# Performance work log

Measured on AMD Instinct MI355X. Metric: run time of the kernel, lower is better.

## Reference

```python
import jax, jax.numpy as jnp
import numpy as np

N = 100_000          # nodes
E = 1_600_000        # edges (avg degree 16)
FEAT = 128           # num_features
HID = 128            # hidden_dim
CLS = 10             # num_classes
G = 4                # grid_size (num RBF grids)
L = 3                # gnn_layers
NG = 64              # number of graphs in batch
GRID_MIN, GRID_MAX = -2.0, 2.0
DENOM = (GRID_MAX - GRID_MIN) / (G - 1)
GRID = jnp.linspace(GRID_MIN, GRID_MAX, G)
LN_EPS = 1e-5


def _layernorm(x, scale, bias):
    m = jnp.mean(x, axis=-1, keepdims=True)
    v = jnp.var(x, axis=-1, keepdims=True)
    return (x - m) * jax.lax.rsqrt(v + LN_EPS) * scale + bias


def _fkan(x, ln_s, ln_b, sW, sb, bW, bb):
    # FastKANLayer: spline_linear(rbf(layernorm(x)).flatten) + base_linear(silu(x))
    z = _layernorm(x, ln_s, ln_b)
    basis = jnp.exp(-(((z[..., None] - GRID) / DENOM) ** 2))      # [n, in, G]
    spline = basis.reshape(x.shape[0], -1) @ sW.T + sb            # [n, out]
    base = jax.nn.silu(x) @ bW.T + bb                             # [n, out]
    return spline + base


def setup_inputs() -> dict:
    key = jax.random.key(0)
    ks = jax.random.split(key, 20)
    inp = {
        "x": jax.random.normal(ks[0], (N, FEAT), dtype=jnp.float32),
        "edge_index": jax.random.randint(ks[1], (2, E), 0, N, dtype=jnp.int64 if jax.config.jax_enable_x64 else jnp.int32),
        "batch": jnp.sort(jax.random.randint(ks[2], (N,), 0, NG)),
        # per-GCN-layer FKAN params (in=out=128 for all 3 layers)
        "ln_s": jnp.ones((L, FEAT), jnp.float32),
        "ln_b": jnp.zeros((L, FEAT), jnp.float32),
        "sW": jax.random.normal(ks[3], (L, HID, FEAT * G), jnp.float32) * 0.05,
        "sb": jnp.zeros((L, HID), jnp.float32),
        "bW": jax.random.normal(ks[4], (L, HID, FEAT), jnp.float32) * 0.05,
        "bb": jnp.zeros((L, HID), jnp.float32),
        "gcn_b": jnp.zeros((L, HID), jnp.float32),
        # readout FastKAN: single FastKANLayer 128 -> 10
        "ro_ln_s": jnp.ones((HID,), jnp.float32),
        "ro_ln_b": jnp.zeros((HID,), jnp.float32),
        "ro_sW": jax.random.normal(ks[5], (CLS, HID * G), jnp.float32) * 0.05,
        "ro_sb": jnp.zeros((CLS,), jnp.float32),
        "ro_bW": jax.random.normal(ks[6], (CLS, HID), jnp.float32) * 0.05,
        "ro_bb": jnp.zeros((CLS,), jnp.float32),
    }
    return inp


def reference(x, edge_index, batch, ln_s, ln_b, sW, sb, bW, bb, gcn_b,
              ro_ln_s, ro_ln_b, ro_sW, ro_sb, ro_bW, ro_bb):
    n = x.shape[0]
    loops = jnp.arange(n, dtype=edge_index.dtype)
    src = jnp.concatenate([edge_index[0], loops])   # with self-loops (GCNConv default)
    dst = jnp.concatenate([edge_index[1], loops])
    deg = jax.ops.segment_sum(jnp.ones_like(src, dtype=x.dtype), dst, num_segments=n)
    dinv = jnp.where(deg > 0, jax.lax.rsqrt(deg), 0.0)
    norm = dinv[src] * dinv[dst]                    # [E+N]

    for i in range(L):
        h = _fkan(x, ln_s[i], ln_b[i], sW[i], sb[i], bW[i], bb[i])    # KAN transform
        agg = jax.ops.segment_sum(norm[:, None] * h[src], dst, num_segments=n)
        x = jax.nn.silu(agg + gcn_b[i])             # dropout p=0 -> identity

    cnt = jax.ops.segment_sum(jnp.ones((n,), x.dtype), batch, num_segments=NG)
    pooled = jax.ops.segment_sum(x, batch, num_segments=NG) / jnp.maximum(cnt, 1.0)[:, None]
    out = _fkan(pooled, ro_ln_s, ro_ln_b, ro_sW, ro_sb, ro_bW, ro_bb)
    return jax.nn.log_softmax(out, axis=1)
```

## Files before the change

### kernel.cpp

```cpp
#include <hip/hip_runtime.h>
#include <math.h>

#define NN     100000
#define NE     1600000
#define FEAT   128
#define GQ     4
#define NL     3
#define NGR    64
#define NCLS   10
#define KSPL   512
#define NKS    10
#define BM     32
#define NB     1563
#define NCHUNK 256
#define CHUNK  6250
#define TILE   1024
#define NT     ((NN + TILE - 1) / TILE)
#define WSTRIDE (NKS*8*2*512)

typedef __attribute__((ext_vector_type(8))) short short8;
typedef __attribute__((ext_vector_type(4))) float floatx4;
typedef __attribute__((ext_vector_type(4))) uint uintx4;

__device__ __forceinline__ float fsilu(float x){ return x / (1.f + __expf(-x)); }
__device__ __forceinline__ ushort f2bf(float f){
  uint u = __builtin_bit_cast(uint, f);
  return (ushort)((u + 0x7FFFu + ((u >> 16) & 1u)) >> 16);
}
__device__ __forceinline__ float bf2f(ushort h){ return __builtin_bit_cast(float, ((uint)h) << 16); }
__device__ __forceinline__ uint bu(float f){ return __builtin_bit_cast(uint, f); }
__device__ __forceinline__ uint pkbf(float lo, float hi){
  return __builtin_amdgcn_perm(bu(hi), bu(lo), 0x07060302u);
}

__global__ __launch_bounds__(256) void k_zero_i(int* __restrict__ p, int n){
  int i = blockIdx.x*256 + threadIdx.x; if (i < n) p[i] = 0;
}
__global__ __launch_bounds__(256) void k_zero_f(float* __restrict__ p, int n){
  int i = blockIdx.x*256 + threadIdx.x; if (i < n) p[i] = 0.f;
}
__global__ __launch_bounds__(256) void k_hist(const int* __restrict__ dst, int* __restrict__ hist, int ne){
  int e = blockIdx.x*256 + threadIdx.x; if (e < ne) atomicAdd(&hist[dst[e]], 1);
}

__global__ __launch_bounds__(256) void k_scan_a(const int* __restrict__ hist, int* __restrict__ tsum){
  __shared__ int red[4];
  const int base = blockIdx.x * TILE;
  int s = 0;
  #pragma unroll
  for (int j = 0; j < 4; ++j){
    int idx = base + threadIdx.x + j*256;
    if (idx < NN) s += hist[idx];
  }
  #pragma unroll
  for (int off = 32; off; off >>= 1) s += __shfl_down(s, off);
  if ((threadIdx.x & 63) == 0) red[threadIdx.x >> 6] = s;
  __syncthreads();
  if (threadIdx.x == 0) tsum[blockIdx.x] = red[0] + red[1] + red[2] + red[3];
}

__global__ __launch_bounds__(128) void k_scan_b(const int* __restrict__ tsum,
                                                int* __restrict__ toff, int* __restrict__ rpN){
  __shared__ int lds[128];
  const int tid = threadIdx.x;
  int v = (tid < NT) ? tsum[tid] : 0;
  lds[tid] = v; __syncthreads();
  for (int off = 1; off < 128; off <<= 1){
    int u = (tid >= off) ? lds[tid - off] : 0;
    __syncthreads();
    lds[tid] += u;
    __syncthreads();
  }
  if (tid < NT) toff[tid] = lds[tid] - v;
  if (tid == NT - 1) *rpN = lds[tid];
}

__global__ __launch_bounds__(256) void k_scan_c(const int* __restrict__ hist,
                                                const int* __restrict__ toff,
                                                int* __restrict__ rp,
                                                float* __restrict__ dinv){
  __shared__ int lds[256];
  const int tid = threadIdx.x;
  const int base = blockIdx.x * TILE + tid*4;
  int h[4]; int s = 0;
  #pragma unroll
  for (int j = 0; j < 4; ++j){ int idx = base + j; h[j] = (idx < NN) ? hist[idx] : 0; s += h[j]; }
  lds[tid] = s; __syncthreads();
  for (int off = 1; off < 256; off <<= 1){
    int u = (tid >= off) ? lds[tid - off] : 0;
    __syncthreads();
    lds[tid] += u;
    __syncthreads();
  }
  int run = toff[blockIdx.x] + lds[tid] - s;
  #pragma unroll
  for (int j = 0; j < 4; ++j){
    int idx = base + j;
    if (idx < NN){
      rp[idx] = run; run += h[j];
      dinv[idx] = rsqrtf((float)h[j] + 1.f);
    }
  }
}

__global__ __launch_bounds__(256) void k_binA(const int* __restrict__ src, const int* __restrict__ dst,
                                              uint* __restrict__ priv, int* __restrict__ seg){
  __shared__ int hist[NB];
  __shared__ int cur[NB];
  __shared__ int scanbuf[256];
  const int c = blockIdx.x, tid = threadIdx.x;
  const size_t e0 = (size_t)c * CHUNK;
  for (int i = tid; i < NB; i += 256) hist[i] = 0;
  __syncthreads();
  for (int i = tid; i < CHUNK; i += 256) atomicAdd(&hist[dst[e0+i] >> 6], 1);
  __syncthreads();
  int loc[7]; int s = 0;
  const int base = tid * 7;
  #pragma unroll
  for (int j = 0; j < 7; ++j){ int idx = base+j; int v = (idx < NB) ? hist[idx] : 0; loc[j] = s; s += v; }
  scanbuf[tid] = s;
  __syncthreads();
  for (int off = 1; off < 256; off <<= 1){
    int u = (tid >= off) ? scanbuf[tid-off] : 0;
    __syncthreads();
    scanbuf[tid] += u;
    __syncthreads();
  }
  const int run = scanbuf[tid] - s;
  #pragma unroll
  for (int j = 0; j < 7; ++j){
    int idx = base+j;
    if (idx < NB){ int st = run + loc[j]; seg[c*(NB+1)+idx] = st; cur[idx] = st; }
  }
  if (tid == 0) seg[c*(NB+1)+NB] = CHUNK;
  __syncthreads();
  for (int i = tid; i < CHUNK; i += 256){
    const uint ss = (uint)src[e0+i], dd = (uint)dst[e0+i];
    const int p = atomicAdd(&cur[dd >> 6], 1);
    priv[(size_t)c*CHUNK + p] = (ss << 6) | (dd & 63u);
  }
}

__global__ __launch_bounds__(256) void k_gathE2(const uint* __restrict__ priv, const int* __restrict__ seg,
                                                const int* __restrict__ rp, int* __restrict__ col){
  __shared__ int cur[64];
  const int b = blockIdx.x, tid = threadIdx.x;
  const int n0 = b * 64;
  if (tid < 64){
    const int idx = n0 + tid;
    cur[tid] = rp[(idx < NN) ? idx : NN];
  }
  __syncthreads();
  const int c = tid;
  const int s0 = seg[c*(NB+1) + b], s1 = seg[c*(NB+1) + b + 1];
  const size_t pbase = (size_t)c*CHUNK;
  for (int i = s0; i < s1; ++i){
    const uint e = priv[pbase + i];
    const int p = atomicAdd(&cur[e & 63u], 1);
    col[p] = (int)(e >> 6);
  }
}

__global__ __launch_bounds__(256) void k_wprep(const float* __restrict__ sW, const float* __restrict__ bW,
                                               ushort* __restrict__ wimg){
  int idx = blockIdx.x*256 + threadIdx.x;
  if (idx >= NL*WSTRIDE) return;
  const int j    = idx & 7;
  const int lane = (idx >> 3) & 63;
  const int ks   = (idx >> 9) & 1;
  const int nr   = (idx >> 10) & 7;
  const int qq   = (idx >> 13) % NKS;
  const int l    = idx / (NKS << 13);
  const int colc = nr*16 + (lane & 15);
  const int kg   = qq*64 + ks*32 + (lane >> 4)*8 + j;
  const float v  = (kg < KSPL) ? sW[((size_t)l*FEAT + colc)*KSPL + kg]
                               : bW[((size_t)l*FEAT + colc)*FEAT + (kg - KSPL)];
  wimg[idx] = f2bf(v);
}

template <typename TIn>
__global__ __launch_bounds__(128) void k_fkan(
    const TIn* __restrict__ xin,
    const ushort* __restrict__ wimg,
    const float* __restrict__ ln_s, const float* __restrict__ ln_b,
    const float* __restrict__ sb, const float* __restrict__ bb,
    const float* __restrict__ dinv,
    ushort* __restrict__ hprime)
{
  __shared__ char xb[BM*256];
  __shared__ float lnS[128], lnB[128], sbias[128];

  const int tid  = threadIdx.x;
  const int lane = tid & 63, wv = tid >> 6;
  const int node0 = blockIdx.x * BM;

  lnS[tid] = ln_s[tid]; lnB[tid] = ln_b[tid]; sbias[tid] = sb[tid] + bb[tid];

  const int lm = tid >> 2, part = tid & 3;
  const int node = node0 + lm;
  const uint swl = ((uint)(lm & 7)) << 4;
  char* xrow_w = xb + lm*256;
  float s1 = 0.f, s2 = 0.f;
  if constexpr (sizeof(TIn) == 4){
    const float4* xr = (const float4*)((const float*)xin + (size_t)node*FEAT + part*32);
    #pragma unroll
    for (int j = 0; j < 4; ++j){
      const float4 a = xr[2*j], b = xr[2*j+1];
      s1 += a.x+a.y+a.z+a.w + b.x+b.y+b.z+b.w;
      s2 += a.x*a.x+a.y*a.y+a.z*a.z+a.w*a.w + b.x*b.x+b.y*b.y+b.z*b.z+b.w*b.w;
      uintx4 pk;
      pk.x = pkbf(a.x, a.y); pk.y = pkbf(a.z, a.w);
      pk.z = pkbf(b.x, b.y); pk.w = pkbf(b.z, b.w);
      *(uintx4*)(xrow_w + (((uint)(part*64 + j*16)) ^ swl)) = pk;
    }
  } else {
    const uintx4* xr = (const uintx4*)((const ushort*)xin + (size_t)node*FEAT + part*32);
    #pragma unroll
    for (int j = 0; j < 4; ++j){
      const uintx4 v = xr[j];
      #pragma unroll
      for (int w = 0; w < 4; ++w){
        const float f0 = bf2f((ushort)(v[w] & 0xffff)), f1 = bf2f((ushort)(v[w] >> 16));
        s1 += f0 + f1; s2 += f0*f0 + f1*f1;
      }
      *(uintx4*)(xrow_w + (((uint)(part*64 + j*16)) ^ swl)) = v;
    }
  }
  s1 += __shfl_xor(s1, 1); s2 += __shfl_xor(s2, 1);
  s1 += __shfl_xor(s1, 2); s2 += __shfl_xor(s2, 2);
  const float mean = s1 * (1.f/128.f);
  const float var  = s2 * (1.f/128.f) - mean*mean;
  const float rsv  = rsqrtf(var + 1e-5f);
  __syncthreads();

  const int l15 = lane & 15, l4h = lane >> 4;
  const int row = wv*16 + l15;
  const uint swz = ((uint)(row & 7)) << 4;
  const char* xrow = xb + row*256;
  const float mrow = __shfl(mean, (lane & 15) << 2);
  const float rrow = __shfl(rsv,  (lane & 15) << 2);

  floatx4 acc[8];
  #pragma unroll
  for (int nr = 0; nr < 8; ++nr){ floatx4 z4 = {0.f,0.f,0.f,0.f}; acc[nr] = z4; }

  const short8* w8 = (const short8*)wimg;

  auto afrag = [&](int sp)->short8 {
    const int q = sp >> 1, ks = sp & 1;
    if (q < 8){
      const int f0 = q*16 + ks*8 + l4h*2;
      const uint xx = *(const uint*)(xrow + (((uint)(f0*2)) ^ swz));
      const float x0 = bf2f((ushort)(xx & 0xffff)), x1 = bf2f((ushort)(xx >> 16));
      const float2 ls = *(const float2*)(lnS + f0);
      const float2 lb = *(const float2*)(lnB + f0);
      const float z0 = (x0 - mrow)*rrow*ls.x + lb.x;
      const float z1 = (x1 - mrow)*rrow*ls.y + lb.y;
      float e0[4], e1[4];
      #pragma unroll
      for (int g = 0; g < 4; ++g){
        const float gc = -2.f + (4.f/3.f)*(float)g;
        const float t0 = (z0 - gc)*0.75f;
        const float t1 = (z1 - gc)*0.75f;
        e0[g] = __expf(-t0*t0);
        e1[g] = __expf(-t1*t1);
      }
      uintx4 pw;
      pw.x = pkbf(e0[0], e0[1]); pw.y = pkbf(e0[2], e0[3]);
      pw.z = pkbf(e1[0], e1[1]); pw.w = pkbf(e1[2], e1[3]);
      return __builtin_bit_cast(short8, pw);
    } else {
      const int f0 = (q - 8)*64 + ks*32 + l4h*8;
      const uintx4 xx = *(const uintx4*)(xrow + (((uint)(f0*2)) ^ swz));
      uintx4 pw;
      #pragma unroll
      for (int w = 0; w < 4; ++w){
        const float x0 = bf2f((ushort)(xx[w] & 0xffff)), x1 = bf2f((ushort)(xx[w] >> 16));
        pw[w] = pkbf(fsilu(x0), fsilu(x1));
      }
      return __builtin_bit_cast(short8, pw);
    }
  };

  short8 b0[8], b1[8];
  #pragma unroll
  for (int nr = 0; nr < 8; ++nr) b0[nr] = w8[(size_t)(nr*2)*64 + lane];

  #pragma unroll
  for (int sp = 0; sp < 20; sp += 2){
    {
      const int q1 = (sp + 1) >> 1, ks1 = (sp + 1) & 1;
      #pragma unroll
      for (int nr = 0; nr < 8; ++nr) b1[nr] = w8[(size_t)(q1*16 + nr*2 + ks1)*64 + lane];
    }
    {
      const short8 af = afrag(sp);
      #pragma unroll
      for (int nr = 0; nr < 8; ++nr)
        acc[nr] = __builtin_amdgcn_mfma_f32_16x16x32_bf16(af, b0[nr], acc[nr], 0, 0, 0);
    }
    if (sp + 2 < 20){
      const int q2 = (sp + 2) >> 1, ks2 = (sp + 2) & 1;
      #pragma unroll
      for (int nr = 0; nr < 8; ++nr) b0[nr] = w8[(size_t)(q2*16 + nr*2 + ks2)*64 + lane];
    }
    {
      const short8 af = afrag(sp + 1);
      #pragma unroll
      for (int nr = 0; nr < 8; ++nr)
        acc[nr] = __builtin_amdgcn_mfma_f32_16x16x32_bf16(af, b1[nr], acc[nr], 0, 0, 0);
    }
  }

  const int rbase = node0 + wv*16 + l4h*4;
  float dvv[4];
  #pragma unroll
  for (int j = 0; j < 4; ++j) dvv[j] = dinv[rbase + j];
  #pragma unroll
  for (int nr = 0; nr < 8; ++nr){
    const int cf = nr*16 + l15;
    const float sv = sbias[cf];
    #pragma unroll
    for (int j = 0; j < 4; ++j)
      hprime[(size_t)(rbase + j)*FEAT + cf] = f2bf(dvv[j]*(acc[nr][j] + sv));
  }
}

__global__ __launch_bounds__(256) void k_aggD(
    const ushort* __restrict__ hprime, const int* __restrict__ rp,
    const int* __restrict__ col, const float* __restrict__ dinv,
    const float* __restrict__ gb, ushort* __restrict__ xout)
{
  const int wv = threadIdx.x >> 6, lane = threadIdx.x & 63;
  const int d = blockIdx.x*4 + wv;
  if (d >= NN) return;
  const uint* h2 = (const uint*)hprime;
  const uint v = h2[(size_t)d*64 + lane];
  float a0 = bf2f((ushort)(v & 0xffff)), a1 = bf2f((ushort)(v >> 16));
  const int j0 = rp[d], j1 = rp[d+1];
  int j = j0;
  for (; j + 7 < j1; j += 8){
    uint w[8];
    #pragma unroll
    for (int u = 0; u < 8; ++u) w[u] = h2[(size_t)col[j+u]*64 + lane];
    #pragma unroll
    for (int u = 0; u < 8; ++u){
      a0 += bf2f((ushort)(w[u] & 0xffff));
      a1 += bf2f((ushort)(w[u] >> 16));
    }
  }
  for (; j + 3 < j1; j += 4){
    uint w[4];
    #pragma unroll
    for (int u = 0; u < 4; ++u) w[u] = h2[(size_t)col[j+u]*64 + lane];
    #pragma unroll
    for (int u = 0; u < 4; ++u){
      a0 += bf2f((ushort)(w[u] & 0xffff));
      a1 += bf2f((ushort)(w[u] >> 16));
    }
  }
  for (; j < j1; ++j){
    const uint w = h2[(size_t)col[j]*64 + lane];
    a0 += bf2f((ushort)(w & 0xffff)); a1 += bf2f((ushort)(w >> 16));
  }
  const float dv = dinv[d];
  const float2 b2 = *(const float2*)(gb + 2*lane);
  a0 = fsilu(dv*a0 + b2.x);
  a1 = fsilu(dv*a1 + b2.y);
  ((uint*)xout)[(size_t)d*64 + lane] = (uint)f2bf(a0) | ((uint)f2bf(a1) << 16);
}

__global__ __launch_bounds__(128) void k_pool(const ushort* __restrict__ x,
                                              const int* __restrict__ batch,
                                              float* __restrict__ pooled,
                                              float* __restrict__ cnt, int n){
  const int f = threadIdx.x;
  const int start = blockIdx.x * 64;
  const int end   = min(start + 64, n);
  if (start >= end) return;
  int cur = batch[start];
  float acc = 0.f, c = 0.f;
  for (int i = start; i < end; ++i){
    const int b = batch[i];
    if (b != cur){
      atomicAdd(&pooled[(size_t)cur*FEAT + f], acc);
      if (f == 0) atomicAdd(&cnt[cur], c);
      cur = b; acc = 0.f; c = 0.f;
    }
    acc += bf2f(x[(size_t)i*FEAT + f]);
    c += 1.f;
  }
  atomicAdd(&pooled[(size_t)cur*FEAT + f], acc);
  if (f == 0) atomicAdd(&cnt[cur], c);
}

__global__ __launch_bounds__(128) void k_pool_div(float* __restrict__ pooled,
                                                  const float* __restrict__ cnt){
  const int g = blockIdx.x, f = threadIdx.x;
  pooled[(size_t)g*FEAT + f] /= fmaxf(cnt[g], 1.f);
}

__global__ __launch_bounds__(128) void k_readout(const float* __restrict__ pooled,
    const float* __restrict__ ln_s, const float* __restrict__ ln_b,
    const float* __restrict__ sW, const float* __restrict__ sb,
    const float* __restrict__ bW, const float* __restrict__ bb,
    float* __restrict__ out){
  __shared__ float cb[KSPL + FEAT];
  __shared__ float wred[2][2];
  __shared__ float outv[NCLS];
  const int tid = threadIdx.x, lane = tid & 63, wave = tid >> 6;
  const int g = blockIdx.x;

  const float xvv = pooled[(size_t)g*FEAT + tid];
  float s1 = xvv, s2 = xvv*xvv;
  #pragma unroll
  for (int off = 32; off; off >>= 1){ s1 += __shfl_down(s1, off); s2 += __shfl_down(s2, off); }
  if (lane == 0){ wred[wave][0] = s1; wred[wave][1] = s2; }
  __syncthreads();
  const float m   = (wred[0][0] + wred[1][0]) * (1.f/FEAT);
  const float var = (wred[0][1] + wred[1][1]) * (1.f/FEAT) - m*m;
  const float rs  = rsqrtf(var + 1e-5f);
  const float z   = (xvv - m) * rs * ln_s[tid] + ln_b[tid];
  #pragma unroll
  for (int gg = 0; gg < GQ; ++gg){
    const float t = (z - (-2.f + (4.f/3.f)*(float)gg)) * 0.75f;
    cb[tid*GQ + gg] = __expf(-t*t);
  }
  cb[KSPL + tid] = fsilu(xvv);
  __syncthreads();

  if (tid < NCLS){
    const float* wr = sW + (size_t)tid*KSPL;
    const float* br = bW + (size_t)tid*FEAT;
    float acc = sb[tid] + bb[tid];
    for (int k = 0; k < KSPL; ++k) acc += cb[k] * wr[k];
    for (int k = 0; k < FEAT; ++k) acc += cb[KSPL + k] * br[k];
    outv[tid] = acc;
  }
  __syncthreads();
  if (tid == 0){
    float mx = -1e30f;
    for (int o = 0; o < NCLS; ++o) mx = fmaxf(mx, outv[o]);
    float se = 0.f;
    for (int o = 0; o < NCLS; ++o) se += __expf(outv[o] - mx);
    const float lse = mx + logf(se);
    for (int o = 0; o < NCLS; ++o) out[(size_t)g*NCLS + o] = outv[o] - lse;
  }
}

extern "C" void kernel_launch(void* const* d_in, const int* in_sizes, int n_in,
                              void* d_out, int out_size, void* d_ws, size_t ws_size,
                              hipStream_t stream) {
  const float* x     = (const float*)d_in[0];
  const int*   edge  = (const int*)d_in[1];
  const int*   batch = (const int*)d_in[2];
  const float* ln_s  = (const float*)d_in[3];
  const float* ln_b  = (const float*)d_in[4];
  const float* sW    = (const float*)d_in[5];
  const float* sb    = (const float*)d_in[6];
  const float* bW    = (const float*)d_in[7];
  const float* bb    = (const float*)d_in[8];
  const float* gcn_b = (const float*)d_in[9];
  const float* ro_ln_s = (const float*)d_in[10];
  const float* ro_ln_b = (const float*)d_in[11];
  const float* ro_sW   = (const float*)d_in[12];
  const float* ro_sb   = (const float*)d_in[13];
  const float* ro_bW   = (const float*)d_in[14];
  const float* ro_bb   = (const float*)d_in[15];
  float* out = (float*)d_out;

  const int* src = edge;
  const int* dst = edge + NE;

  char* W = (char*)d_ws;
  size_t off = 0;
  auto alloc = [&](size_t bytes){ size_t r = off; off += (bytes + 1023) & ~((size_t)1023); return r; };
  float*  dinv   = (float*) (W + alloc((size_t)NN*4));
  ushort* wimg   = (ushort*)(W + alloc((size_t)NL*WSTRIDE*2));
  int*    hist   = (int*)   (W + alloc((size_t)NN*4));
  int*    rp     = (int*)   (W + alloc((size_t)(NN+1)*4));
  int*    tsum   = (int*)   (W + alloc((size_t)NT*4));
  int*    toff   = (int*)   (W + alloc((size_t)NT*4));
  uint*   priv   = (uint*)  (W + alloc((size_t)NE*4));
  int*    seg    = (int*)   (W + alloc((size_t)NCHUNK*(NB+1)*4));
  int*    col    = (int*)   (W + alloc((size_t)NE*4));
  ushort* hprime = (ushort*)(W + alloc((size_t)NN*FEAT*2));
  ushort* xcur   = (ushort*)(W + alloc((size_t)NN*FEAT*2));
  float*  pooled = (float*) (W + alloc((size_t)(NGR*FEAT + NGR)*4));
  float*  cnt    = pooled + NGR*FEAT;

  k_zero_i<<<(NN+255)/256, 256, 0, stream>>>(hist, NN);
  k_zero_f<<<(NGR*FEAT+NGR+255)/256, 256, 0, stream>>>(pooled, NGR*FEAT + NGR);
  k_hist<<<(NE+255)/256, 256, 0, stream>>>(dst, hist, NE);
  k_scan_a<<<NT, 256, 0, stream>>>(hist, tsum);
  k_scan_b<<<1, 128, 0, stream>>>(tsum, toff, rp + NN);
  k_scan_c<<<NT, 256, 0, stream>>>(hist, toff, rp, dinv);
  k_binA<<<NCHUNK, 256, 0, stream>>>(src, dst, priv, seg);
  k_gathE2<<<NB, 256, 0, stream>>>(priv, seg, rp, col);
  k_wprep<<<(NL*WSTRIDE + 255)/256, 256, 0, stream>>>(sW, bW, wimg);

  const int fkan_grid = NN / BM;
  for (int l = 0; l < NL; ++l){
    const ushort* wl = wimg + (size_t)l*WSTRIDE;
    if (l == 0)
      k_fkan<float><<<fkan_grid, 128, 0, stream>>>(x, wl,
          ln_s + l*FEAT, ln_b + l*FEAT, sb + l*FEAT, bb + l*FEAT, dinv, hprime);
    else
      k_fkan<ushort><<<fkan_grid, 128, 0, stream>>>(xcur, wl,
          ln_s + l*FEAT, ln_b + l*FEAT, sb + l*FEAT, bb + l*FEAT, dinv, hprime);
    k_aggD<<<(NN+3)/4, 256, 0, stream>>>(hprime, rp, col, dinv, gcn_b + l*FEAT, xcur);
  }

  k_pool<<<(NN+63)/64, 128, 0, stream>>>(xcur, batch, pooled, cnt, NN);
  k_pool_div<<<NGR, 128, 0, stream>>>(pooled, cnt);
  k_readout<<<NGR, 128, 0, stream>>>(pooled, ro_ln_s, ro_ln_b,
                                     ro_sW, ro_sb, ro_bW, ro_bb, out);
}
```

Measured before the change: 490.3 us.

## Stage FKAN weight fragments in LDS via async global_load_lds with larger node tiles

The FKAN kernel now processes 64 nodes per block with 256 threads. Each wave previously loaded all weight fragments from global memory on its own; now the block loads them cooperatively into a double-buffered LDS stage using global_load_lds, and every wave reads them from LDS. The goal is to cut redundant global and L2 weight traffic and to share it across four waves. The cost is a __syncthreads on every k-step and an unrolled loop that has become a rolled one, which may serialize the MFMA pipeline. Bounds checks are added for the partial last tile.

```diff
diff --git a/kernel.cpp b/kernel.cpp
--- a/kernel.cpp
+++ b/kernel.cpp
@@ -10,7 +10,7 @@
 #define NCLS   10
 #define KSPL   512
 #define NKS    10
-#define BM     32
+#define BM     64
 #define NB     1563
 #define NCHUNK 256
 #define CHUNK  6250
@@ -31,6 +31,11 @@
 __device__ __forceinline__ uint bu(float f){ return __builtin_bit_cast(uint, f); }
 __device__ __forceinline__ uint pkbf(float lo, float hi){
   return __builtin_amdgcn_perm(bu(hi), bu(lo), 0x07060302u);
+}
+__device__ __forceinline__ void gld_lds16(const ushort* g, ushort* l){
+  __builtin_amdgcn_global_load_lds(
+      (const __attribute__((address_space(1))) uint*)g,
+      (__attribute__((address_space(3))) uint*)l, 16, 0, 0);
 }
 
 __global__ __launch_bounds__(256) void k_zero_i(int* __restrict__ p, int n){
@@ -179,7 +184,7 @@
 }
 
 template <typename TIn>
-__global__ __launch_bounds__(128) void k_fkan(
+__global__ __launch_bounds__(256) void k_fkan(
     const TIn* __restrict__ xin,
     const ushort* __restrict__ wimg,
     const float* __restrict__ ln_s, const float* __restrict__ ln_b,
@@ -188,63 +193,87 @@
     ushort* __restrict__ hprime)
 {
   __shared__ char xb[BM*256];
+  __shared__ ushort Bst[2][8*512];
   __shared__ float lnS[128], lnB[128], sbias[128];
 
   const int tid  = threadIdx.x;
   const int lane = tid & 63, wv = tid >> 6;
   const int node0 = blockIdx.x * BM;
 
-  lnS[tid] = ln_s[tid]; lnB[tid] = ln_b[tid]; sbias[tid] = sb[tid] + bb[tid];
+  if (tid < 128){ lnS[tid] = ln_s[tid]; lnB[tid] = ln_b[tid]; sbias[tid] = sb[tid] + bb[tid]; }
 
   const int lm = tid >> 2, part = tid & 3;
   const int node = node0 + lm;
   const uint swl = ((uint)(lm & 7)) << 4;
   char* xrow_w = xb + lm*256;
   float s1 = 0.f, s2 = 0.f;
-  if constexpr (sizeof(TIn) == 4){
-    const float4* xr = (const float4*)((const float*)xin + (size_t)node*FEAT + part*32);
-    #pragma unroll
-    for (int j = 0; j < 4; ++j){
-      const float4 a = xr[2*j], b = xr[2*j+1];
-      s1 += a.x+a.y+a.z+a.w + b.x+b.y+b.z+b.w;
-      s2 += a.x*a.x+a.y*a.y+a.z*a.z+a.w*a.w + b.x*b.x+b.y*b.y+b.z*b.z+b.w*b.w;
-      uintx4 pk;
-      pk.x = pkbf(a.x, a.y); pk.y = pkbf(a.z, a.w);
-      pk.z = pkbf(b.x, b.y); pk.w = pkbf(b.z, b.w);
-      *(uintx4*)(xrow_w + (((uint)(part*64 + j*16)) ^ swl)) = pk;
+  if (node < NN){
+    if constexpr (sizeof(TIn) == 4){
+      const float4* xr = (const float4*)((const float*)xin + (size_t)node*FEAT + part*32);
+      #pragma unroll
+      for (int j = 0; j < 4; ++j){
+        const float4 a = xr[2*j], b = xr[2*j+1];
+        s1 += a.x+a.y+a.z+a.w + b.x+b.y+b.z+b.w;
+        s2 += a.x*a.x+a.y*a.y+a.z*a.z+a.w*a.w + b.x*b.x+b.y*b.y+b.z*b.z+b.w*b.w;
+        uintx4 pk;
+        pk.x = pkbf(a.x, a.y); pk.y = pkbf(a.z, a.w);
+        pk.z = pkbf(b.x, b.y); pk.w = pkbf(b.z, b.w);
+        *(uintx4*)(xrow_w + (((uint)(part*64 + j*16)) ^ swl)) = pk;
+      }
+    } else {
+      const uintx4* xr = (const uintx4*)((const ushort*)xin + (size_t)node*FEAT + part*32);
+      #pragma unroll
+      for (int j = 0; j < 2; ++j){
+        const uintx4 v = xr[j];
+        #pragma unroll
+        for (int w = 0; w < 4; ++w){
+          const float f0 = bf2f((ushort)(v[w] & 0xffff)), f1 = bf2f((ushort)(v[w] >> 16));
+          s1 += f0 + f1; s2 += f0*f0 + f1*f1;
+        }
+        *(uintx4*)(xrow_w + (((uint)(part*64 + j*16)) ^ swl)) = v;
+      }
+      #pragma unroll
+      for (int j = 2; j < 4; ++j){
+        const uintx4 v = xr[j];
+        #pragma unroll
+        for (int w = 0; w < 4; ++w){
+          const float f0 = bf2f((ushort)(v[w] & 0xffff)), f1 = bf2f((ushort)(v[w] >> 16));
+          s1 += f0 + f1; s2 += f0*f0 + f1*f1;
+        }
+        *(uintx4*)(xrow_w + (((uint)(part*64 + j*16)) ^ swl)) = v;
+      }
     }
   } else {
-    const uintx4* xr = (const uintx4*)((const ushort*)xin + (size_t)node*FEAT + part*32);
-    #pragma unroll
-    for (int j = 0; j < 4; ++j){
-      const uintx4 v = xr[j];
-      #pragma unroll
-      for (int w = 0; w < 4; ++w){
-        const float f0 = bf2f((ushort)(v[w] & 0xffff)), f1 = bf2f((ushort)(v[w] >> 16));
-        s1 += f0 + f1; s2 += f0*f0 + f1*f1;
-      }
-      *(uintx4*)(xrow_w + (((uint)(part*64 + j*16)) ^ swl)) = v;
-    }
+    uintx4 z4 = {0u,0u,0u,0u};
+    #pragma unroll
+    for (int j = 0; j < 4; ++j)
+      *(uintx4*)(xrow_w + (((uint)(part*64 + j*16)) ^ swl)) = z4;
   }
   s1 += __shfl_xor(s1, 1); s2 += __shfl_xor(s2, 1);
   s1 += __shfl_xor(s1, 2); s2 += __shfl_xor(s2, 2);
   const float mean = s1 * (1.f/128.f);
   const float var  = s2 * (1.f/128.f) - mean*mean;
   const float rsv  = rsqrtf(var + 1e-5f);
+
+  {
+    #pragma unroll
+    for (int f = 0; f < 2; ++f){
+      const int nr = (wv << 1) | f;
+      gld_lds16(wimg + ((size_t)(nr*2) << 9) + (lane << 3), &Bst[0][nr << 9]);
+    }
+  }
   __syncthreads();
 
   const int l15 = lane & 15, l4h = lane >> 4;
   const int row = wv*16 + l15;
   const uint swz = ((uint)(row & 7)) << 4;
   const char* xrow = xb + row*256;
-  const float mrow = __shfl(mean, (lane & 15) << 2);
-  const float rrow = __shfl(rsv,  (lane & 15) << 2);
+  const float mrow = __shfl(mean, l15 << 2);
+  const float rrow = __shfl(rsv,  l15 << 2);
 
   floatx4 acc[8];
   #pragma unroll
   for (int nr = 0; nr < 8; ++nr){ floatx4 z4 = {0.f,0.f,0.f,0.f}; acc[nr] = z4; }
-
-  const short8* w8 = (const short8*)wimg;
 
   auto afrag = [&](int sp)->short8 {
     const int q = sp >> 1, ks = sp & 1;
@@ -282,47 +311,41 @@
     }
   };
 
-  short8 b0[8], b1[8];
-  #pragma unroll
-  for (int nr = 0; nr < 8; ++nr) b0[nr] = w8[(size_t)(nr*2)*64 + lane];
-
-  #pragma unroll
-  for (int sp = 0; sp < 20; sp += 2){
-    {
+  for (int sp = 0; sp < 20; ++sp){
+    if (sp + 1 < 20){
       const int q1 = (sp + 1) >> 1, ks1 = (sp + 1) & 1;
       #pragma unroll
-      for (int nr = 0; nr < 8; ++nr) b1[nr] = w8[(size_t)(q1*16 + nr*2 + ks1)*64 + lane];
-    }
-    {
-      const short8 af = afrag(sp);
-      #pragma unroll
-      for (int nr = 0; nr < 8; ++nr)
-        acc[nr] = __builtin_amdgcn_mfma_f32_16x16x32_bf16(af, b0[nr], acc[nr], 0, 0, 0);
-    }
-    if (sp + 2 < 20){
-      const int q2 = (sp + 2) >> 1, ks2 = (sp + 2) & 1;
-      #pragma unroll
-      for (int nr = 0; nr < 8; ++nr) b0[nr] = w8[(size_t)(q2*16 + nr*2 + ks2)*64 + lane];
-    }
-    {
-      const short8 af = afrag(sp + 1);
-      #pragma unroll
-      for (int nr = 0; nr < 8; ++nr)
-        acc[nr] = __builtin_amdgcn_mfma_f32_16x16x32_bf16(af, b1[nr], acc[nr], 0, 0, 0);
-    }
+      for (int f = 0; f < 2; ++f){
+        const int nr = (wv << 1) | f;
+        gld_lds16(wimg + ((size_t)(q1*16 + nr*2 + ks1) << 9) + (lane << 3),
+                  &Bst[(sp + 1) & 1][nr << 9]);
+      }
+    }
+    const short8 af = afrag(sp);
+    const char* bb_ = (const char*)&Bst[sp & 1][0];
+    short8 bf[8];
+    #pragma unroll
+    for (int nr = 0; nr < 8; ++nr)
+      bf[nr] = *(const short8*)(bb_ + (nr << 10) + (lane << 4));
+    #pragma unroll
+    for (int nr = 0; nr < 8; ++nr)
+      acc[nr] = __builtin_amdgcn_mfma_f32_16x16x32_bf16(af, bf[nr], acc[nr], 0, 0, 0);
+    __syncthreads();
   }
 
   const int rbase = node0 + wv*16 + l4h*4;
   float dvv[4];
   #pragma unroll
-  for (int j = 0; j < 4; ++j) dvv[j] = dinv[rbase + j];
+  for (int j = 0; j < 4; ++j) dvv[j] = (rbase + j < NN) ? dinv[rbase + j] : 0.f;
   #pragma unroll
   for (int nr = 0; nr < 8; ++nr){
     const int cf = nr*16 + l15;
     const float sv = sbias[cf];
     #pragma unroll
-    for (int j = 0; j < 4; ++j)
-      hprime[(size_t)(rbase + j)*FEAT + cf] = f2bf(dvv[j]*(acc[nr][j] + sv));
+    for (int j = 0; j < 4; ++j){
+      const int r = rbase + j;
+      if (r < NN) hprime[(size_t)r*FEAT + cf] = f2bf(dvv[j]*(acc[nr][j] + sv));
+    }
   }
 }
 
@@ -499,14 +522,14 @@
   k_gathE2<<<NB, 256, 0, stream>>>(priv, seg, rp, col);
   k_wprep<<<(NL*WSTRIDE + 255)/256, 256, 0, stream>>>(sW, bW, wimg);
 
-  const int fkan_grid = NN / BM;
+  const int fkan_grid = (NN + BM - 1) / BM;
   for (int l = 0; l < NL; ++l){
     const ushort* wl = wimg + (size_t)l*WSTRIDE;
     if (l == 0)
-      k_fkan<float><<<fkan_grid, 128, 0, stream>>>(x, wl,
+      k_fkan<float><<<fkan_grid, 256, 0, stream>>>(x, wl,
           ln_s + l*FEAT, ln_b + l*FEAT, sb + l*FEAT, bb + l*FEAT, dinv, hprime);
     else
-      k_fkan<ushort><<<fkan_grid, 128, 0, stream>>>(xcur, wl,
+      k_fkan<ushort><<<fkan_grid, 256, 0, stream>>>(xcur, wl,
           ln_s + l*FEAT, ln_b + l*FEAT, sb + l*FEAT, bb + l*FEAT, dinv, hprime);
     k_aggD<<<(NN+3)/4, 256, 0, stream>>>(hprime, rp, col, dinv, gcn_b + l*FEAT, xcur);
   }
```

Measured after the change: 507.6 us. +3.5%, slower.

## Split FKAN GEMM columns across four waves per block and use exp2 for RBF

Applied to the files above, without the earlier changes.

The FKAN kernel block grows from 128 to 256 threads. Each pair of waves now shares a 16-row tile and splits the 128 output columns in half, so each wave holds 4 accumulators and 4 weight fragments instead of 8. Row LayerNorm statistics now go through shared memory instead of lane shuffles. The RBF exponent folds the scale and log2(e) into one constant and calls exp2f. In exchange, each pair of waves computes the A fragments (basis and silu) twice, which is meant to be offset by lower register pressure and higher occupancy.

```diff
diff --git a/kernel.cpp b/kernel.cpp
--- a/kernel.cpp
+++ b/kernel.cpp
@@ -179,7 +179,7 @@
 }
 
 template <typename TIn>
-__global__ __launch_bounds__(128) void k_fkan(
+__global__ __launch_bounds__(256) void k_fkan(
     const TIn* __restrict__ xin,
     const ushort* __restrict__ wimg,
     const float* __restrict__ ln_s, const float* __restrict__ ln_b,
@@ -188,63 +188,69 @@
     ushort* __restrict__ hprime)
 {
   __shared__ char xb[BM*256];
+  __shared__ float2 rstat[BM];
   __shared__ float lnS[128], lnB[128], sbias[128];
 
   const int tid  = threadIdx.x;
   const int lane = tid & 63, wv = tid >> 6;
   const int node0 = blockIdx.x * BM;
 
-  lnS[tid] = ln_s[tid]; lnB[tid] = ln_b[tid]; sbias[tid] = sb[tid] + bb[tid];
-
-  const int lm = tid >> 2, part = tid & 3;
+  if (tid < 128){ lnS[tid] = ln_s[tid]; lnB[tid] = ln_b[tid]; sbias[tid] = sb[tid] + bb[tid]; }
+
+  const int lm = tid >> 3, part = tid & 7;
   const int node = node0 + lm;
   const uint swl = ((uint)(lm & 7)) << 4;
   char* xrow_w = xb + lm*256;
   float s1 = 0.f, s2 = 0.f;
   if constexpr (sizeof(TIn) == 4){
-    const float4* xr = (const float4*)((const float*)xin + (size_t)node*FEAT + part*32);
-    #pragma unroll
-    for (int j = 0; j < 4; ++j){
+    const float4* xr = (const float4*)((const float*)xin + (size_t)node*FEAT + part*16);
+    #pragma unroll
+    for (int j = 0; j < 2; ++j){
       const float4 a = xr[2*j], b = xr[2*j+1];
       s1 += a.x+a.y+a.z+a.w + b.x+b.y+b.z+b.w;
       s2 += a.x*a.x+a.y*a.y+a.z*a.z+a.w*a.w + b.x*b.x+b.y*b.y+b.z*b.z+b.w*b.w;
       uintx4 pk;
       pk.x = pkbf(a.x, a.y); pk.y = pkbf(a.z, a.w);
       pk.z = pkbf(b.x, b.y); pk.w = pkbf(b.z, b.w);
-      *(uintx4*)(xrow_w + (((uint)(part*64 + j*16)) ^ swl)) = pk;
+      *(uintx4*)(xrow_w + (((uint)(part*32 + j*16)) ^ swl)) = pk;
     }
   } else {
-    const uintx4* xr = (const uintx4*)((const ushort*)xin + (size_t)node*FEAT + part*32);
-    #pragma unroll
-    for (int j = 0; j < 4; ++j){
+    const uintx4* xr = (const uintx4*)((const ushort*)xin + (size_t)node*FEAT + part*16);
+    #pragma unroll
+    for (int j = 0; j < 2; ++j){
       const uintx4 v = xr[j];
       #pragma unroll
       for (int w = 0; w < 4; ++w){
         const float f0 = bf2f((ushort)(v[w] & 0xffff)), f1 = bf2f((ushort)(v[w] >> 16));
         s1 += f0 + f1; s2 += f0*f0 + f1*f1;
       }
-      *(uintx4*)(xrow_w + (((uint)(part*64 + j*16)) ^ swl)) = v;
+      *(uintx4*)(xrow_w + (((uint)(part*32 + j*16)) ^ swl)) = v;
     }
   }
   s1 += __shfl_xor(s1, 1); s2 += __shfl_xor(s2, 1);
   s1 += __shfl_xor(s1, 2); s2 += __shfl_xor(s2, 2);
-  const float mean = s1 * (1.f/128.f);
-  const float var  = s2 * (1.f/128.f) - mean*mean;
-  const float rsv  = rsqrtf(var + 1e-5f);
+  s1 += __shfl_xor(s1, 4); s2 += __shfl_xor(s2, 4);
+  if (part == 0){
+    const float mean = s1 * (1.f/128.f);
+    const float var  = s2 * (1.f/128.f) - mean*mean;
+    rstat[lm] = make_float2(mean, rsqrtf(var + 1e-5f));
+  }
   __syncthreads();
 
   const int l15 = lane & 15, l4h = lane >> 4;
-  const int row = wv*16 + l15;
+  const int rg = wv >> 1, wn = wv & 1;
+  const int row = rg*16 + l15;
   const uint swz = ((uint)(row & 7)) << 4;
   const char* xrow = xb + row*256;
-  const float mrow = __shfl(mean, (lane & 15) << 2);
-  const float rrow = __shfl(rsv,  (lane & 15) << 2);
-
-  floatx4 acc[8];
-  #pragma unroll
-  for (int nr = 0; nr < 8; ++nr){ floatx4 z4 = {0.f,0.f,0.f,0.f}; acc[nr] = z4; }
+  const float2 st = rstat[row];
+  const float mrow = st.x, rrow = st.y;
+
+  floatx4 acc[4];
+  #pragma unroll
+  for (int nr = 0; nr < 4; ++nr){ floatx4 z4 = {0.f,0.f,0.f,0.f}; acc[nr] = z4; }
 
   const short8* w8 = (const short8*)wimg;
+  const int nbase = wn*4;
 
   auto afrag = [&](int sp)->short8 {
     const int q = sp >> 1, ks = sp & 1;
@@ -256,14 +262,14 @@
       const float2 lb = *(const float2*)(lnB + f0);
       const float z0 = (x0 - mrow)*rrow*ls.x + lb.x;
       const float z1 = (x1 - mrow)*rrow*ls.y + lb.y;
+      const float C = -0.81152344f;
       float e0[4], e1[4];
       #pragma unroll
       for (int g = 0; g < 4; ++g){
         const float gc = -2.f + (4.f/3.f)*(float)g;
-        const float t0 = (z0 - gc)*0.75f;
-        const float t1 = (z1 - gc)*0.75f;
-        e0[g] = __expf(-t0*t0);
-        e1[g] = __expf(-t1*t1);
+        const float d0 = z0 - gc, d1 = z1 - gc;
+        e0[g] = exp2f(d0*d0*C);
+        e1[g] = exp2f(d1*d1*C);
       }
       uintx4 pw;
       pw.x = pkbf(e0[0], e0[1]); pw.y = pkbf(e0[2], e0[3]);
@@ -282,47 +288,50 @@
     }
   };
 
-  short8 b0[8], b1[8];
-  #pragma unroll
-  for (int nr = 0; nr < 8; ++nr) b0[nr] = w8[(size_t)(nr*2)*64 + lane];
+  short8 b0[4], b1[4];
+  #pragma unroll
+  for (int nrl = 0; nrl < 4; ++nrl)
+    b0[nrl] = w8[(size_t)((nbase + nrl)*2)*64 + lane];
 
   #pragma unroll
   for (int sp = 0; sp < 20; sp += 2){
     {
       const int q1 = (sp + 1) >> 1, ks1 = (sp + 1) & 1;
       #pragma unroll
-      for (int nr = 0; nr < 8; ++nr) b1[nr] = w8[(size_t)(q1*16 + nr*2 + ks1)*64 + lane];
+      for (int nrl = 0; nrl < 4; ++nrl)
+        b1[nrl] = w8[(size_t)(q1*16 + (nbase + nrl)*2 + ks1)*64 + lane];
     }
     {
       const short8 af = afrag(sp);
       #pragma unroll
-      for (int nr = 0; nr < 8; ++nr)
-        acc[nr] = __builtin_amdgcn_mfma_f32_16x16x32_bf16(af, b0[nr], acc[nr], 0, 0, 0);
+      for (int nrl = 0; nrl < 4; ++nrl)
+        acc[nrl] = __builtin_amdgcn_mfma_f32_16x16x32_bf16(af, b0[nrl], acc[nrl], 0, 0, 0);
     }
     if (sp + 2 < 20){
       const int q2 = (sp + 2) >> 1, ks2 = (sp + 2) & 1;
       #pragma unroll
-      for (int nr = 0; nr < 8; ++nr) b0[nr] = w8[(size_t)(q2*16 + nr*2 + ks2)*64 + lane];
+      for (int nrl = 0; nrl < 4; ++nrl)
+        b0[nrl] = w8[(size_t)(q2*16 + (nbase + nrl)*2 + ks2)*64 + lane];
     }
     {
       const short8 af = afrag(sp + 1);
       #pragma unroll
-      for (int nr = 0; nr < 8; ++nr)
-        acc[nr] = __builtin_amdgcn_mfma_f32_16x16x32_bf16(af, b1[nr], acc[nr], 0, 0, 0);
-    }
-  }
-
-  const int rbase = node0 + wv*16 + l4h*4;
+      for (int nrl = 0; nrl < 4; ++nrl)
+        acc[nrl] = __builtin_amdgcn_mfma_f32_16x16x32_bf16(af, b1[nrl], acc[nrl], 0, 0, 0);
+    }
+  }
+
+  const int rbase = node0 + rg*16 + l4h*4;
   float dvv[4];
   #pragma unroll
   for (int j = 0; j < 4; ++j) dvv[j] = dinv[rbase + j];
   #pragma unroll
-  for (int nr = 0; nr < 8; ++nr){
-    const int cf = nr*16 + l15;
+  for (int nrl = 0; nrl < 4; ++nrl){
+    const int cf = wn*64 + nrl*16 + l15;
     const float sv = sbias[cf];
     #pragma unroll
     for (int j = 0; j < 4; ++j)
-      hprime[(size_t)(rbase + j)*FEAT + cf] = f2bf(dvv[j]*(acc[nr][j] + sv));
+      hprime[(size_t)(rbase + j)*FEAT + cf] = f2bf(dvv[j]*(acc[nrl][j] + sv));
   }
 }
 
@@ -503,10 +512,10 @@
   for (int l = 0; l < NL; ++l){
     const ushort* wl = wimg + (size_t)l*WSTRIDE;
     if (l == 0)
-      k_fkan<float><<<fkan_grid, 128, 0, stream>>>(x, wl,
+      k_fkan<float><<<fkan_grid, 256, 0, stream>>>(x, wl,
           ln_s + l*FEAT, ln_b + l*FEAT, sb + l*FEAT, bb + l*FEAT, dinv, hprime);
     else
-      k_fkan<ushort><<<fkan_grid, 128, 0, stream>>>(xcur, wl,
+      k_fkan<ushort><<<fkan_grid, 256, 0, stream>>>(xcur, wl,
           ln_s + l*FEAT, ln_b + l*FEAT, sb + l*FEAT, bb + l*FEAT, dinv, hprime);
     k_aggD<<<(NN+3)/4, 256, 0, stream>>>(hprime, rp, col, dinv, gcn_b + l*FEAT, xcur);
   }
```

New measurement: 529.6 us. 1.08x slower.
